# Performance work log

Measured on AMD Instinct MI355X. Metric: run time of the kernel, lower is better.

Reference implementation:

```python
import jax, jax.numpy as jnp
import numpy as np
import math

B, Hdim, Wdim, C = 8, 64, 64, 512
T, TXT = 77, 512
NH, HD = 8, 64  # num_heads, head_dim
TOP_M = 3
CLAMP_LOGIT = 2.0
CONF_THRESH = 0.35
NEG_INF = -1e30


def _ln(x, g, b, eps=1e-5):
    mu = x.mean(-1, keepdims=True)
    var = ((x - mu) ** 2).mean(-1, keepdims=True)
    return (x - mu) * jax.lax.rsqrt(var + eps) * g + b


def _l2norm(x, eps=1e-6):
    n = jnp.sqrt((x * x).sum(-1, keepdims=True))
    return x / jnp.maximum(n, eps)


def setup_inputs() -> dict:
    key = jax.random.key(0)
    ks = jax.random.split(key, 16)
    s = 0.02
    inp = {
        'visual_features': jax.random.normal(ks[0], (B, Hdim, Wdim, C), jnp.float32),
        'text_features': jax.random.normal(ks[1], (B, T, TXT), jnp.float32),
        'ln1_g': jnp.ones((C,), jnp.float32), 'ln1_b': jnp.zeros((C,), jnp.float32),
        'ln2_g': jnp.ones((C,), jnp.float32), 'ln2_b': jnp.zeros((C,), jnp.float32),
        'Wq': jax.random.normal(ks[2], (C, C), jnp.float32) * s, 'bq': jnp.zeros((C,), jnp.float32),
        'Wk': jax.random.normal(ks[3], (TXT, C), jnp.float32) * s, 'bk': jnp.zeros((C,), jnp.float32),
        'Wv': jax.random.normal(ks[4], (TXT, C), jnp.float32) * s, 'bv': jnp.zeros((C,), jnp.float32),
        'Wo': jax.random.normal(ks[5], (C, C), jnp.float32) * s, 'bo': jnp.zeros((C,), jnp.float32),
        'Wg': jax.random.normal(ks[6], (C, 1), jnp.float32) * s, 'bg': jnp.zeros((1,), jnp.float32),
        'W1': jax.random.normal(ks[7], (C, 4 * C), jnp.float32) * s, 'b1': jnp.zeros((4 * C,), jnp.float32),
        'W2': jax.random.normal(ks[8], (4 * C, C), jnp.float32) * s, 'b2': jnp.zeros((C,), jnp.float32),
        'logit_scale': jnp.asarray(math.log(1.0 / 0.07), jnp.float32),
        'alpha': jnp.asarray(0.1, jnp.float32),
    }
    return inp


def reference(visual_features, text_features, ln1_g, ln1_b, ln2_g, ln2_b,
              Wq, bq, Wk, bk, Wv, bv, Wo, bo, Wg, bg, W1, b1, W2, b2,
              logit_scale, alpha):
    b, h, w, c = visual_features.shape
    n = h * w
    # Pre-LN on visual tokens
    x = _ln(visual_features, ln1_g, ln1_b).reshape(b, n, c)
    q_full = x @ Wq + bq                                   # [B,N,C]
    pad_mask = jnp.abs(text_features).sum(-1) <= 1e-6      # [B,T]
    k_full = text_features @ Wk + bk                       # [B,T,C]
    v_full = text_features @ Wv + bv
    # l2-normalize over full channel dim, then split heads
    q = _l2norm(q_full).reshape(b, n, NH, HD)
    k = _l2norm(k_full).reshape(b, T, NH, HD)
    v = v_full.reshape(b, T, NH, HD)
    scale = jnp.exp(jnp.clip(logit_scale, -CLAMP_LOGIT, CLAMP_LOGIT)) / math.sqrt(float(HD))
    sim = jnp.einsum('bnhd,bthd->bnht', q, k) * scale      # [B,N,H,T]
    sim = jnp.where(pad_mask[:, None, None, :], NEG_INF, sim)
    # top-k sparsification: keep top_m per (b,n,h) row
    topv = jax.lax.top_k(sim, TOP_M)[0][..., -1:]
    sim = jnp.where(sim >= topv, sim, NEG_INF)
    attn = jax.nn.softmax(sim, axis=-1)
    attn = attn / jnp.maximum(attn.sum(-1, keepdims=True), 1e-6)
    all_pad = pad_mask.all(axis=1)                         # [B]
    attn = jnp.where(all_pad[:, None, None, None], 0.0, attn)
    # confidence: max-prob * (1 - normalized entropy), mean over heads
    attn_hn = attn.transpose(0, 2, 1, 3)                   # [B,H,N,T]
    maxp = attn_hn.max(-1, keepdims=True)
    t_eff = jnp.maximum((attn_hn > 0).astype(jnp.float32).sum(-1, keepdims=True), 2.0)
    p = jnp.maximum(attn_hn, 1e-8)
    entropy = jnp.maximum(-(p * jnp.log(p)).sum(-1, keepdims=True) / jnp.log(t_eff), 0.0)
    conf = jnp.clip(maxp * (1.0 - entropy), 0.0, 1.0).mean(axis=1)  # [B,N,1]
    bypass = (conf >= CONF_THRESH).astype(attn.dtype)
    aligned = jnp.einsum('bnht,bthd->bnhd', attn, v).reshape(b, n, c)
    aligned = (aligned @ Wo + bo) * bypass
    gate = jax.nn.sigmoid(x @ Wg + bg)                     # [B,N,1]
    y = x + alpha * gate * aligned
    y = _ln(y, ln2_g, ln2_b)
    y = y + (jax.nn.gelu(y @ W1 + b1, approximate=False) @ W2 + b2)
    return y.reshape(b, h, w, c)
```

## Files before the change

### kernel.cpp

```cpp
#include <hip/hip_runtime.h>
#include <stdint.h>

#define BATCH 8
#define NTOK 4096
#define CDIM 512
#define TTXT 77
#define TPAD 80
#define NHEAD 8
#define HDIM 64
#define HID 2048
#define MROWS 32768
#define NEGINF (-1e30f)

typedef __attribute__((ext_vector_type(8))) short short8;
typedef __attribute__((ext_vector_type(4))) float f32x4;

__device__ __forceinline__ float b2f(unsigned short u) {
    union { unsigned int i; float f; } x; x.i = ((unsigned int)u) << 16; return x.f;
}
__device__ __forceinline__ unsigned short f2b(float f) {
    union { float f; unsigned int i; } x; x.f = f;
    unsigned int i = x.i;
    return (unsigned short)((i + 0x7fffu + ((i >> 16) & 1u)) >> 16);
}

__device__ __forceinline__ void gload16(const void* g, void* l) {
    __builtin_amdgcn_global_load_lds(
        (const __attribute__((address_space(1))) unsigned int*)g,
        (__attribute__((address_space(3))) unsigned int*)l, 16, 0, 0);
}

#define OFF_WQT   ((size_t)0)
#define OFF_WKT   (OFF_WQT + 512*512*2)
#define OFF_WVT   (OFF_WKT + 512*512*2)
#define OFF_WOT   (OFF_WVT + 512*512*2)
#define OFF_W1T   (OFF_WOT + 512*512*2)
#define OFF_W2T   (OFF_W1T + (size_t)2048*512*2)
#define OFF_TEXTB (OFF_W2T + (size_t)512*2048*2)
#define OFF_KFB   (OFF_TEXTB + (size_t)640*512*2)
#define OFF_KNRM  (OFF_KFB + (size_t)640*512*2)
#define OFF_VPAD  (OFF_KNRM + (size_t)640*512*2)
#define OFF_PADM  (OFF_VPAD + (size_t)640*512*2)
#define OFF_ALLP  (OFF_PADM + 2560)
#define OFF_GATE  (OFF_ALLP + 256)
#define OFF_BYP   (OFF_GATE + (size_t)MROWS*4)
#define OFF_XB    (OFF_BYP + (size_t)MROWS*4)
#define OFF_BUFB  (OFF_XB + (size_t)MROWS*CDIM*2)
#define OFF_BUFC  (OFF_BUFB + (size_t)MROWS*CDIM*2)
#define OFF_H     (OFF_BUFC + (size_t)MROWS*CDIM*2)
#define WS_NEED   (OFF_H + (size_t)MROWS*HID*2)
#define OFF_VT    OFF_H

__device__ __forceinline__ float waveReduceAdd(float v) {
#pragma unroll
    for (int m = 1; m < 64; m <<= 1) v += __shfl_xor(v, m);
    return v;
}
__device__ __forceinline__ float waveReduceMin(float v) {
#pragma unroll
    for (int m = 1; m < 64; m <<= 1) v = fminf(v, __shfl_xor(v, m));
    return v;
}
__device__ __forceinline__ float red16Max(float v) {
#pragma unroll
    for (int m = 1; m < 16; m <<= 1) v = fmaxf(v, __shfl_xor(v, m));
    return v;
}
__device__ __forceinline__ float red16Add(float v) {
#pragma unroll
    for (int m = 1; m < 16; m <<= 1) v += __shfl_xor(v, m);
    return v;
}

__global__ __launch_bounds__(256) void transpose_kernel(
    const float* __restrict__ in, unsigned short* __restrict__ out, int R, int C)
{
    __shared__ float tile[32][33];
    const int tx = threadIdx.x & 31, ty = threadIdx.x >> 5;
    const int c0 = blockIdx.x * 32, r0 = blockIdx.y * 32;
#pragma unroll
    for (int i = 0; i < 32; i += 8)
        tile[ty + i][tx] = in[(size_t)(r0 + ty + i) * C + c0 + tx];
    __syncthreads();
#pragma unroll
    for (int i = 0; i < 32; i += 8)
        out[(size_t)(c0 + ty + i) * R + r0 + tx] = f2b(tile[tx][ty + i]);
}

__global__ __launch_bounds__(128) void text_prep_kernel(
    const float* __restrict__ text, unsigned short* __restrict__ textb, float* __restrict__ padm)
{
    __shared__ float sred[2];
    const int r = blockIdx.x;
    const int b = r / TPAD, t = r % TPAD;
    const int tid = threadIdx.x;
    if (t < TTXT) {
        float4 v = *(const float4*)(text + ((size_t)(b * TTXT + t)) * 512 + tid * 4);
        float a = fabsf(v.x) + fabsf(v.y) + fabsf(v.z) + fabsf(v.w);
        a = waveReduceAdd(a);
        if ((tid & 63) == 0) sred[tid >> 6] = a;
        __syncthreads();
        float asum = sred[0] + sred[1];
        ushort4 o; o.x = f2b(v.x); o.y = f2b(v.y); o.z = f2b(v.z); o.w = f2b(v.w);
        *(ushort4*)(textb + (size_t)r * 512 + tid * 4) = o;
        if (tid == 0) padm[r] = (asum <= 1e-6f) ? 1.f : 0.f;
    } else {
        ushort4 z; z.x = 0; z.y = 0; z.z = 0; z.w = 0;
        *(ushort4*)(textb + (size_t)r * 512 + tid * 4) = z;
        if (tid == 0) padm[r] = 1.f;
    }
}

__global__ __launch_bounds__(128) void allpad_kernel(
    const float* __restrict__ padm, float* __restrict__ allp)
{
    __shared__ float sred[2];
    const int b = blockIdx.x, tid = threadIdx.x;
    float f = (tid < TTXT) ? padm[b * TPAD + tid] : 1.f;
    f = waveReduceMin(f);
    if ((tid & 63) == 0) sred[tid >> 6] = f;
    __syncthreads();
    if (tid == 0) allp[b] = fminf(sred[0], sred[1]);
}

__global__ __launch_bounds__(128) void ln1_gate_kernel(
    const float* __restrict__ vin, const float* __restrict__ g1, const float* __restrict__ b1v,
    const float* __restrict__ Wg, const float* __restrict__ bg,
    unsigned short* __restrict__ xb, float* __restrict__ gate)
{
    __shared__ float sred[4];
    const int row = blockIdx.x, tid = threadIdx.x;
    const float4 v = *(const float4*)(vin + (size_t)row * 512 + tid * 4);
    float s = v.x + v.y + v.z + v.w;
    float s2 = v.x * v.x + v.y * v.y + v.z * v.z + v.w * v.w;
    s = waveReduceAdd(s); s2 = waveReduceAdd(s2);
    if ((tid & 63) == 0) { sred[tid >> 6] = s; sred[2 + (tid >> 6)] = s2; }
    __syncthreads();
    s = sred[0] + sred[1]; s2 = sred[2] + sred[3];
    const float mu = s * (1.f / 512.f);
    float var = s2 * (1.f / 512.f) - mu * mu;
    const float rs = rsqrtf(fmaxf(var, 0.f) + 1e-5f);
    const float4 gg = *(const float4*)(g1 + tid * 4);
    const float4 bb = *(const float4*)(b1v + tid * 4);
    const float x0 = (v.x - mu) * rs * gg.x + bb.x;
    const float x1 = (v.y - mu) * rs * gg.y + bb.y;
    const float x2 = (v.z - mu) * rs * gg.z + bb.z;
    const float x3 = (v.w - mu) * rs * gg.w + bb.w;
    ushort4 o; o.x = f2b(x0); o.y = f2b(x1); o.z = f2b(x2); o.w = f2b(x3);
    *(ushort4*)(xb + (size_t)row * 512 + tid * 4) = o;
    const float4 wg = *(const float4*)(Wg + tid * 4);
    float gp = x0 * wg.x + x1 * wg.y + x2 * wg.z + x3 * wg.w;
    gp = waveReduceAdd(gp);
    __syncthreads();
    if ((tid & 63) == 0) sred[tid >> 6] = gp;
    __syncthreads();
    if (tid == 0) {
        float z = sred[0] + sred[1] + bg[0];
        gate[row] = 1.f / (1.f + __expf(-z));
    }
}

__global__ __launch_bounds__(128) void ln2_kernel(
    const unsigned short* __restrict__ yin, const float* __restrict__ g2, const float* __restrict__ b2v,
    unsigned short* __restrict__ yb)
{
    __shared__ float sred[4];
    const int row = blockIdx.x, tid = threadIdx.x;
    ushort4 u = *(const ushort4*)(yin + (size_t)row * 512 + tid * 4);
    float v0 = b2f(u.x), v1 = b2f(u.y), v2 = b2f(u.z), v3 = b2f(u.w);
    float s = v0 + v1 + v2 + v3;
    float s2 = v0 * v0 + v1 * v1 + v2 * v2 + v3 * v3;
    s = waveReduceAdd(s); s2 = waveReduceAdd(s2);
    if ((tid & 63) == 0) { sred[tid >> 6] = s; sred[2 + (tid >> 6)] = s2; }
    __syncthreads();
    s = sred[0] + sred[1]; s2 = sred[2] + sred[3];
    const float mu = s * (1.f / 512.f);
    float var = s2 * (1.f / 512.f) - mu * mu;
    const float rs = rsqrtf(fmaxf(var, 0.f) + 1e-5f);
    const float4 gg = *(const float4*)(g2 + tid * 4);
    const float4 bb = *(const float4*)(b2v + tid * 4);
    ushort4 o;
    o.x = f2b((v0 - mu) * rs * gg.x + bb.x);
    o.y = f2b((v1 - mu) * rs * gg.y + bb.y);
    o.z = f2b((v2 - mu) * rs * gg.z + bb.z);
    o.w = f2b((v3 - mu) * rs * gg.w + bb.w);
    *(ushort4*)(yb + (size_t)row * 512 + tid * 4) = o;
}

__global__ __launch_bounds__(128) void l2norm_kernel(
    const unsigned short* __restrict__ in, unsigned short* __restrict__ out)
{
    __shared__ float sred[2];
    const int row = blockIdx.x, tid = threadIdx.x;
    ushort4 u = *(const ushort4*)(in + (size_t)row * 512 + tid * 4);
    float v0 = b2f(u.x), v1 = b2f(u.y), v2 = b2f(u.z), v3 = b2f(u.w);
    float ss = v0 * v0 + v1 * v1 + v2 * v2 + v3 * v3;
    ss = waveReduceAdd(ss);
    if ((tid & 63) == 0) sred[tid >> 6] = ss;
    __syncthreads();
    ss = sred[0] + sred[1];
    const float inv = 1.f / fmaxf(sqrtf(ss), 1e-6f);
    ushort4 o;
    o.x = f2b(v0 * inv); o.y = f2b(v1 * inv); o.z = f2b(v2 * inv); o.w = f2b(v3 * inv);
    *(ushort4*)(out + (size_t)row * 512 + tid * 4) = o;
}

__global__ __launch_bounds__(256) void vt_prep_kernel(
    const unsigned short* __restrict__ vp, unsigned short* __restrict__ vt)
{
    __shared__ unsigned short st[80][72];
    const int b = blockIdx.x >> 3, h = blockIdx.x & 7;
    const int tid = threadIdx.x;
    for (int idx = tid; idx < 80 * 64; idx += 256) {
        int t = idx >> 6, d = idx & 63;
        st[t][d] = vp[((size_t)(b * TPAD + t)) * 512 + h * 64 + d];
    }
    __syncthreads();
    for (int idx = tid; idx < 64 * 96; idx += 256) {
        int d = idx / 96, t = idx - d * 96;
        vt[((size_t)blockIdx.x * 64 + d) * 96 + t] = (t < TPAD) ? st[t][d] : (unsigned short)0;
    }
}

__global__ __launch_bounds__(256) void gemm_bt(
    const unsigned short* __restrict__ A, const unsigned short* __restrict__ Bt,
    const float* __restrict__ bias,
    unsigned short* __restrict__ outb, int M, int N, int K)
{
    __shared__ unsigned short sA[128 * 64];
    __shared__ unsigned short sB[128 * 64];
    char* cA = (char*)sA;
    char* cB = (char*)sB;
    const int tid = threadIdx.x;
    const int lane = tid & 63, w = tid >> 6;
    const int g = lane >> 4, ln = lane & 15;
    const int WR = w >> 1, WC = w & 1;
    const int rowA0 = blockIdx.x * 128, colB0 = blockIdx.y * 128;

    f32x4 acc[4][4];
#pragma unroll
    for (int m = 0; m < 4; ++m)
#pragma unroll
        for (int n = 0; n < 4; ++n) acc[m][n] = (f32x4){0.f, 0.f, 0.f, 0.f};

    for (int k0 = 0; k0 < K; k0 += 64) {
        __syncthreads();
#pragma unroll
        for (int i = 0; i < 4; ++i) {
            int c = tid + i * 256;
            int row = c >> 3, kc = c & 7;
            int kcs = kc ^ (row & 7);
            gload16(A + (size_t)(rowA0 + row) * K + k0 + kcs * 8, cA + c * 16);
            gload16(Bt + (size_t)(colB0 + row) * K + k0 + kcs * 8, cB + c * 16);
        }
        __syncthreads();
#pragma unroll
        for (int kk = 0; kk < 2; ++kk) {
            short8 af[4], bf[4];
#pragma unroll
            for (int m = 0; m < 4; ++m) {
                int row = WR * 64 + m * 16 + ln;
                af[m] = *(const short8*)(cA + row * 128 + ((kk * 64 + g * 16) ^ ((row & 7) << 4)));
            }
#pragma unroll
            for (int n = 0; n < 4; ++n) {
                int col = WC * 64 + n * 16 + ln;
                bf[n] = *(const short8*)(cB + col * 128 + ((kk * 64 + g * 16) ^ ((col & 7) << 4)));
            }
#pragma unroll
            for (int m = 0; m < 4; ++m)
#pragma unroll
                for (int n = 0; n < 4; ++n)
                    acc[m][n] = __builtin_amdgcn_mfma_f32_16x16x32_bf16(af[m], bf[n], acc[m][n], 0, 0, 0);
        }
    }

#pragma unroll
    for (int m = 0; m < 4; ++m) {
        const int rbase = rowA0 + WR * 64 + m * 16 + g * 4;
#pragma unroll
        for (int n = 0; n < 4; ++n) {
            const int col = colB0 + WC * 64 + n * 16 + ln;
            const float bcol = bias[col];
#pragma unroll
            for (int i = 0; i < 4; ++i)
                outb[(size_t)(rbase + i) * N + col] = f2b(acc[m][n][i] + bcol);
        }
    }
}

template<int EPI>
__global__ __launch_bounds__(512, 2) void gemm256(
    const unsigned short* __restrict__ A, const unsigned short* __restrict__ Bt,
    const float* __restrict__ bias,
    unsigned short* __restrict__ outb, float* __restrict__ outf,
    int M, int N, int K,
    const unsigned short* __restrict__ xres, const float* __restrict__ gate,
    const float* __restrict__ byp, const unsigned short* __restrict__ yres,
    const float* __restrict__ alphaPtr, int gxM, int gyN)
{
    __shared__ unsigned short lds[2][2][16384];
    const int tid = threadIdx.x;
    const int lane = tid & 63, w = tid >> 6;
    const int g = lane >> 4, ln = lane & 15;
    const int wr = w >> 2, wc = w & 3;

    int bm, bn;
    {
        const int L = (int)blockIdx.x;
        const int xcd = L & 7, j = L >> 3;
        const int rl = j / gyN;
        bn = j - rl * gyN;
        bm = xcd * (gxM >> 3) + rl;
    }
    const int rowA0 = bm * 256, colB0 = bn * 256;
    const int nt = K >> 6;

    auto stageA = [&](int t, int mh) {
        const int buf = t & 1;
#pragma unroll
        for (int r = 0; r < 2; ++r) {
            const int c = tid + r * 512;
            const int prl = c >> 3, kc = c & 7;
            const int grow = rowA0 + ((prl >> 6) << 7) + (mh << 6) + (prl & 63);
            gload16(A + (size_t)grow * K + (t << 6) + ((kc ^ (prl & 7)) << 3),
                    (char*)&lds[buf][0][mh * 8192] + c * 16);
        }
    };
    auto stageB = [&](int t, int nh) {
        const int buf = t & 1;
#pragma unroll
        for (int r = 0; r < 2; ++r) {
            const int c = tid + r * 512;
            const int prl = c >> 3, kc = c & 7;
            const int gcol = colB0 + ((prl >> 5) << 6) + (nh << 5) + (prl & 31);
            gload16(Bt + (size_t)gcol * K + (t << 6) + ((kc ^ (prl & 7)) << 3),
                    (char*)&lds[buf][1][nh * 8192] + c * 16);
        }
    };

    f32x4 acc[8][4];
#pragma unroll
    for (int m = 0; m < 8; ++m)
#pragma unroll
        for (int n = 0; n < 4; ++n) acc[m][n] = (f32x4){0.f, 0.f, 0.f, 0.f};

    stageA(0, 0); stageB(0, 0); stageB(0, 1); stageA(0, 1);
    stageA(1, 0); stageB(1, 0); stageB(1, 1);
    asm volatile("s_waitcnt vmcnt(6)" ::: "memory");
    __builtin_amdgcn_s_barrier();

    const int sw  = (ln & 7) << 4;
    const int kb0 = (g * 16) ^ sw;
    const int kb1 = (64 + g * 16) ^ sw;
    const int arow = (wr * 64 + ln) * 128;
    const int brow = (wc * 32 + ln) * 128;

    short8 afr[4][2], bfr[4][2];

    for (int t = 0; t < nt; ++t) {
        const char* lA = (const char*)&lds[t & 1][0][0];
        const char* lB = (const char*)&lds[t & 1][1][0];

#pragma unroll
        for (int m = 0; m < 4; ++m) {
            afr[m][0] = *(const short8*)(lA + arow + m * 2048 + kb0);
            afr[m][1] = *(const short8*)(lA + arow + m * 2048 + kb1);
        }
#pragma unroll
        for (int n = 0; n < 2; ++n) {
            bfr[n][0] = *(const short8*)(lB + brow + n * 2048 + kb0);
            bfr[n][1] = *(const short8*)(lB + brow + n * 2048 + kb1);
        }
        if (t + 1 < nt) stageA(t + 1, 1);
        __builtin_amdgcn_s_barrier();
        __builtin_amdgcn_s_setprio(1);
#pragma unroll
        for (int m = 0; m < 4; ++m)
#pragma unroll
            for (int n = 0; n < 2; ++n) {
                acc[m][n] = __builtin_amdgcn_mfma_f32_16x16x32_bf16(afr[m][0], bfr[n][0], acc[m][n], 0, 0, 0);
                acc[m][n] = __builtin_amdgcn_mfma_f32_16x16x32_bf16(afr[m][1], bfr[n][1], acc[m][n], 0, 0, 0);
            }
        __builtin_amdgcn_s_setprio(0);
        __builtin_amdgcn_s_barrier();

#pragma unroll
        for (int n = 2; n < 4; ++n) {
            bfr[n][0] = *(const short8*)(lB + brow + (n & 1) * 2048 + 16384 + kb0);
            bfr[n][1] = *(const short8*)(lB + brow + (n & 1) * 2048 + 16384 + kb1);
        }
        if (t + 2 < nt) stageA(t + 2, 0);
        __builtin_amdgcn_s_barrier();
        __builtin_amdgcn_s_setprio(1);
#pragma unroll
        for (int m = 0; m < 4; ++m)
#pragma unroll
            for (int n = 2; n < 4; ++n) {
                acc[m][n] = __builtin_amdgcn_mfma_f32_16x16x32_bf16(afr[m][0], bfr[n][0], acc[m][n], 0, 0, 0);
                acc[m][n] = __builtin_amdgcn_mfma_f32_16x16x32_bf16(afr[m][1], bfr[n][1], acc[m][n], 0, 0, 0);
            }
        __builtin_amdgcn_s_setprio(0);
        __builtin_amdgcn_s_barrier();

#pragma unroll
        for (int m = 0; m < 4; ++m) {
            afr[m][0] = *(const short8*)(lA + arow + m * 2048 + 16384 + kb0);
            afr[m][1] = *(const short8*)(lA + arow + m * 2048 + 16384 + kb1);
        }
        if (t + 2 < nt) stageB(t + 2, 0);
        __builtin_amdgcn_s_barrier();
        __builtin_amdgcn_s_setprio(1);
#pragma unroll
        for (int m = 0; m < 4; ++m)
#pragma unroll
            for (int n = 0; n < 2; ++n) {
                acc[m + 4][n] = __builtin_amdgcn_mfma_f32_16x16x32_bf16(afr[m][0], bfr[n][0], acc[m + 4][n], 0, 0, 0);
                acc[m + 4][n] = __builtin_amdgcn_mfma_f32_16x16x32_bf16(afr[m][1], bfr[n][1], acc[m + 4][n], 0, 0, 0);
            }
        __builtin_amdgcn_s_setprio(0);
        __builtin_amdgcn_s_barrier();

        if (t + 2 < nt) stageB(t + 2, 1);
        if (t == nt - 2) { asm volatile("s_waitcnt vmcnt(0)" ::: "memory"); }
        else             { asm volatile("s_waitcnt vmcnt(6)" ::: "memory"); }
        __builtin_amdgcn_s_barrier();
        __builtin_amdgcn_s_setprio(1);
#pragma unroll
        for (int m = 0; m < 4; ++m)
#pragma unroll
            for (int n = 2; n < 4; ++n) {
                acc[m + 4][n] = __builtin_amdgcn_mfma_f32_16x16x32_bf16(afr[m][0], bfr[n][0], acc[m + 4][n], 0, 0, 0);
                acc[m + 4][n] = __builtin_amdgcn_mfma_f32_16x16x32_bf16(afr[m][1], bfr[n][1], acc[m + 4][n], 0, 0, 0);
            }
        __builtin_amdgcn_s_setprio(0);
        __builtin_amdgcn_s_barrier();
    }

    const float alpha = (EPI == 1) ? *alphaPtr : 0.f;
#pragma unroll
    for (int m = 0; m < 8; ++m) {
        const int rbase = rowA0 + wr * 128 + m * 16 + g * 4;
#pragma unroll
        for (int n = 0; n < 4; ++n) {
            const int col = colB0 + wc * 64 + n * 16 + ln;
            const float bcol = bias[col];
#pragma unroll
            for (int i = 0; i < 4; ++i) {
                const int row = rbase + i;
                const float v = acc[m][n][i] + bcol;
                if (EPI == 0) {
                    outb[(size_t)row * N + col] = f2b(v);
                } else if (EPI == 1) {
                    float yp = b2f(xres[(size_t)row * N + col]) + alpha * gate[row] * byp[row] * v;
                    outb[(size_t)row * N + col] = f2b(yp);
                } else if (EPI == 2) {
                    const float u2 = 2.f * v * (0.7978845608f + 0.0356774081f * v * v);
                    const float tt = 1.f - 2.f / (__expf(u2) + 1.f);
                    outb[(size_t)row * N + col] = f2b(0.5f * v * (1.f + tt));
                } else {
                    outf[(size_t)row * N + col] = b2f(yres[(size_t)row * N + col]) + v;
                }
            }
        }
    }
}

__global__ __launch_bounds__(256) void attn_kernel(
    const unsigned short* __restrict__ qn,
    const unsigned short* __restrict__ kn,
    const unsigned short* __restrict__ vt,
    const float* __restrict__ padm,
    const float* __restrict__ allp,
    const float* __restrict__ lscPtr,
    unsigned short* __restrict__ aligned,
    float* __restrict__ bypass)
{
    const int b = blockIdx.y;
    const int n0 = blockIdx.x * 16;
    const int tid = threadIdx.x;
    const int w = tid >> 6, lane = tid & 63, g = lane >> 4, ln = lane & 15;
    __shared__ unsigned short s_p[4][16][104];
    __shared__ float s_conf[4][16];

    if (allp[b] > 0.5f) {
        uint4 z = {0u, 0u, 0u, 0u};
#pragma unroll
        for (int j = 0; j < 4; ++j) {
            int id = tid + j * 256;
            int row = id >> 6, c8 = id & 63;
            *(uint4*)(aligned + ((size_t)(b * NTOK + n0 + row)) * 512 + c8 * 8) = z;
        }
        if (tid < 16) bypass[b * NTOK + n0 + tid] = 0.f;
        return;
    }

    float lscale;
    {
        float ls = *lscPtr;
        ls = fminf(fmaxf(ls, -2.f), 2.f);
        lscale = __expf(ls) * 0.125f;
    }

    float pm[5];
#pragma unroll
    for (int tt = 0; tt < 5; ++tt) {
        int t = ln + tt * 16;
        pm[tt] = (t < TTXT) ? padm[b * TPAD + t] : 1.f;
    }

    for (int j = g; j < 24; j += 4) s_p[w][ln][80 + j] = 0;

    float conf_acc[4] = {0.f, 0.f, 0.f, 0.f};
    const size_t qrow = ((size_t)(b * NTOK + n0 + ln)) * 512;

#pragma unroll
    for (int hh = 0; hh < 2; ++hh) {
        const int h = w + hh * 4;
        short8 a0 = *(const short8*)(qn + qrow + h * 64 + g * 8);
        short8 a1 = *(const short8*)(qn + qrow + h * 64 + 32 + g * 8);
        f32x4 sim[5];
#pragma unroll
        for (int tt = 0; tt < 5; ++tt) {
            const size_t kbase = ((size_t)(b * TPAD + tt * 16 + ln)) * 512 + h * 64;
            short8 b0 = *(const short8*)(kn + kbase + g * 8);
            short8 b1 = *(const short8*)(kn + kbase + 32 + g * 8);
            f32x4 c = (f32x4){0.f, 0.f, 0.f, 0.f};
            c = __builtin_amdgcn_mfma_f32_16x16x32_bf16(a0, b0, c, 0, 0, 0);
            c = __builtin_amdgcn_mfma_f32_16x16x32_bf16(a1, b1, c, 0, 0, 0);
            sim[tt] = c;
        }
#pragma unroll
        for (int i = 0; i < 4; ++i) {
            float v[5];
#pragma unroll
            for (int tt = 0; tt < 5; ++tt)
                v[tt] = (pm[tt] == 0.f) ? sim[tt][i] * lscale : NEGINF;

            float lm = v[0];
#pragma unroll
            for (int tt = 1; tt < 5; ++tt) lm = fmaxf(lm, v[tt]);
            const float m1 = red16Max(lm);
            float lm2 = -3.0e38f;
#pragma unroll
            for (int tt = 0; tt < 5; ++tt) if (v[tt] < m1) lm2 = fmaxf(lm2, v[tt]);
            const float m2 = red16Max(lm2);
            float lm3 = -3.0e38f;
#pragma unroll
            for (int tt = 0; tt < 5; ++tt) if (v[tt] < m2) lm3 = fmaxf(lm3, v[tt]);
            const float m3 = red16Max(lm3);
            float lc1 = 0.f, lc2 = 0.f;
#pragma unroll
            for (int tt = 0; tt < 5; ++tt) {
                if (v[tt] >= m1) lc1 += 1.f;
                if (v[tt] >= m2) lc2 += 1.f;
            }
            const float c1 = red16Add(lc1);
            const float c2 = red16Add(lc2);
            const float th = (c1 >= 3.f) ? m1 : ((c2 >= 3.f) ? m2 : m3);

            float p[5], lsum = 0.f, lcnt = 0.f;
#pragma unroll
            for (int tt = 0; tt < 5; ++tt) {
                float pv = (v[tt] >= th) ? __expf(v[tt] - m1) : 0.f;
                p[tt] = pv;
                lsum += pv;
                lcnt += (pv > 0.f) ? 1.f : 0.f;
            }
            const float psum = red16Add(lsum);
            const float pcnt = red16Add(lcnt);
            const float inv = 1.f / fmaxf(psum, 1e-20f);

            float lmaxp = 0.f, lent = 0.f;
#pragma unroll
            for (int tt = 0; tt < 5; ++tt) {
                float a = p[tt] * inv;
                p[tt] = a;
                lmaxp = fmaxf(lmaxp, a);
                if (a > 0.f) {
                    float pp = fmaxf(a, 1e-8f);
                    lent += -pp * __logf(pp);
                }
            }
            const float maxp = red16Max(lmaxp);
            float ent = red16Add(lent);
            ent += (77.f - pcnt) * 1.8420680744e-7f;
            const float teff = fmaxf(pcnt, 2.f);
            const float entropy = fmaxf(ent / __logf(teff), 0.f);
            const float confh = fminf(fmaxf(maxp * (1.f - entropy), 0.f), 1.f);
            conf_acc[i] += confh;

#pragma unroll
            for (int tt = 0; tt < 5; ++tt)
                s_p[w][g * 4 + i][ln + tt * 16] = f2b(p[tt]);
        }
        short8 af[3];
#pragma unroll
        for (int k = 0; k < 3; ++k)
            af[k] = *(const short8*)(&s_p[w][ln][k * 32 + g * 8]);
        const size_t vtb = ((size_t)(b * NHEAD + h)) * 64;
#pragma unroll
        for (int n = 0; n < 4; ++n) {
            f32x4 o = (f32x4){0.f, 0.f, 0.f, 0.f};
#pragma unroll
            for (int k = 0; k < 3; ++k) {
                short8 bf = *(const short8*)(vt + (vtb + n * 16 + ln) * 96 + k * 32 + g * 8);
                o = __builtin_amdgcn_mfma_f32_16x16x32_bf16(af[k], bf, o, 0, 0, 0);
            }
#pragma unroll
            for (int i = 0; i < 4; ++i)
                aligned[((size_t)(b * NTOK + n0 + g * 4 + i)) * 512 + h * 64 + n * 16 + ln] =
                    f2b(o[i]);
        }
    }

    if (ln == 0) {
#pragma unroll
        for (int i = 0; i < 4; ++i) s_conf[w][g * 4 + i] = conf_acc[i];
    }
    __syncthreads();
    if (tid < 16) {
        float c = (s_conf[0][tid] + s_conf[1][tid] + s_conf[2][tid] + s_conf[3][tid]) * 0.125f;
        bypass[b * NTOK + n0 + tid] = (c >= 0.35f) ? 1.f : 0.f;
    }
}

extern "C" void kernel_launch(void* const* d_in, const int* in_sizes, int n_in,
                              void* d_out, int out_size, void* d_ws, size_t ws_size,
                              hipStream_t stream)
{
    (void)in_sizes; (void)n_in; (void)out_size;
    if (ws_size < WS_NEED) return;

    const float* visual = (const float*)d_in[0];
    const float* text   = (const float*)d_in[1];
    const float* ln1_g  = (const float*)d_in[2];
    const float* ln1_b  = (const float*)d_in[3];
    const float* ln2_g  = (const float*)d_in[4];
    const float* ln2_b  = (const float*)d_in[5];
    const float* Wq = (const float*)d_in[6];   const float* bq = (const float*)d_in[7];
    const float* Wk = (const float*)d_in[8];   const float* bk = (const float*)d_in[9];
    const float* Wv = (const float*)d_in[10];  const float* bv = (const float*)d_in[11];
    const float* Wo = (const float*)d_in[12];  const float* bo = (const float*)d_in[13];
    const float* Wg = (const float*)d_in[14];  const float* bg = (const float*)d_in[15];
    const float* W1 = (const float*)d_in[16];  const float* b1 = (const float*)d_in[17];
    const float* W2 = (const float*)d_in[18];  const float* b2 = (const float*)d_in[19];
    const float* lsc = (const float*)d_in[20];
    const float* alp = (const float*)d_in[21];

    char* ws = (char*)d_ws;
    unsigned short* WQT  = (unsigned short*)(ws + OFF_WQT);
    unsigned short* WKT  = (unsigned short*)(ws + OFF_WKT);
    unsigned short* WVT  = (unsigned short*)(ws + OFF_WVT);
    unsigned short* WOT  = (unsigned short*)(ws + OFF_WOT);
    unsigned short* W1T  = (unsigned short*)(ws + OFF_W1T);
    unsigned short* W2T  = (unsigned short*)(ws + OFF_W2T);
    unsigned short* TEXTB = (unsigned short*)(ws + OFF_TEXTB);
    unsigned short* KFB  = (unsigned short*)(ws + OFF_KFB);
    unsigned short* KNRM = (unsigned short*)(ws + OFF_KNRM);
    unsigned short* VPAD = (unsigned short*)(ws + OFF_VPAD);
    float* PADM = (float*)(ws + OFF_PADM);
    float* ALLP = (float*)(ws + OFF_ALLP);
    float* GATE = (float*)(ws + OFF_GATE);
    float* BYP  = (float*)(ws + OFF_BYP);
    unsigned short* XB   = (unsigned short*)(ws + OFF_XB);
    unsigned short* BUFB = (unsigned short*)(ws + OFF_BUFB);
    unsigned short* BUFC = (unsigned short*)(ws + OFF_BUFC);
    unsigned short* HBUF = (unsigned short*)(ws + OFF_H);
    unsigned short* VT   = (unsigned short*)(ws + OFF_VT);
    float* out = (float*)d_out;

    transpose_kernel<<<dim3(16, 16), 256, 0, stream>>>(Wq, WQT, 512, 512);
    transpose_kernel<<<dim3(16, 16), 256, 0, stream>>>(Wk, WKT, 512, 512);
    transpose_kernel<<<dim3(16, 16), 256, 0, stream>>>(Wv, WVT, 512, 512);
    transpose_kernel<<<dim3(16, 16), 256, 0, stream>>>(Wo, WOT, 512, 512);
    transpose_kernel<<<dim3(64, 16), 256, 0, stream>>>(W1, W1T, 512, 2048);
    transpose_kernel<<<dim3(16, 64), 256, 0, stream>>>(W2, W2T, 2048, 512);

    text_prep_kernel<<<640, 128, 0, stream>>>(text, TEXTB, PADM);
    allpad_kernel<<<BATCH, 128, 0, stream>>>(PADM, ALLP);

    ln1_gate_kernel<<<MROWS, 128, 0, stream>>>(visual, ln1_g, ln1_b, Wg, bg, XB, GATE);

    gemm_bt<<<dim3(5, 4), 256, 0, stream>>>(TEXTB, WKT, bk, KFB, 640, 512, 512);
    gemm_bt<<<dim3(5, 4), 256, 0, stream>>>(TEXTB, WVT, bv, VPAD, 640, 512, 512);
    l2norm_kernel<<<640, 128, 0, stream>>>(KFB, KNRM);
    vt_prep_kernel<<<BATCH * NHEAD, 256, 0, stream>>>(VPAD, VT);

    gemm256<0><<<dim3(128 * 2), 512, 0, stream>>>(XB, WQT, bq, BUFB, nullptr, MROWS, 512, 512,
                                                  nullptr, nullptr, nullptr, nullptr, nullptr,
                                                  128, 2);
    l2norm_kernel<<<MROWS, 128, 0, stream>>>(BUFB, BUFC);

    attn_kernel<<<dim3(NTOK / 16, BATCH), 256, 0, stream>>>(BUFC, KNRM, VT, PADM, ALLP, lsc,
                                                            BUFB, BYP);

    gemm256<1><<<dim3(128 * 2), 512, 0, stream>>>(BUFB, WOT, bo, BUFC, nullptr, MROWS, 512, 512,
                                                  XB, GATE, BYP, nullptr, alp, 128, 2);

    ln2_kernel<<<MROWS, 128, 0, stream>>>(BUFC, ln2_g, ln2_b, XB);

    gemm256<2><<<dim3(128 * 8), 512, 0, stream>>>(XB, W1T, b1, HBUF, nullptr, MROWS, HID, 512,
                                                  nullptr, nullptr, nullptr, nullptr, nullptr,
                                                  128, 8);
    gemm256<3><<<dim3(128 * 2), 512, 0, stream>>>(HBUF, W2T, b2, nullptr, out, MROWS, 512, HID,
                                                  nullptr, nullptr, nullptr, XB, nullptr,
                                                  128, 2);
}
```

Measured before the change: 398.5 us.

## Fuse query L2-norm into attention kernel and merge weight transposes

```diff
diff --git a/kernel.cpp b/kernel.cpp
--- a/kernel.cpp
+++ b/kernel.cpp
@@ -72,19 +72,34 @@
     return v;
 }
 
-__global__ __launch_bounds__(256) void transpose_kernel(
-    const float* __restrict__ in, unsigned short* __restrict__ out, int R, int C)
+__global__ __launch_bounds__(256) void transpose_all_kernel(
+    const float* __restrict__ Wq, const float* __restrict__ Wk,
+    const float* __restrict__ Wv, const float* __restrict__ Wo,
+    const float* __restrict__ W1, const float* __restrict__ W2,
+    unsigned short* __restrict__ WQT, unsigned short* __restrict__ WKT,
+    unsigned short* __restrict__ WVT, unsigned short* __restrict__ WOT,
+    unsigned short* __restrict__ W1T, unsigned short* __restrict__ W2T)
 {
     __shared__ float tile[32][33];
+    int b = blockIdx.x;
+    const float* src; unsigned short* dst; int R, C, cx, ry;
+    if (b < 1024)       { src = W1; dst = W1T; R = 512;  C = 2048; cx = b & 63; ry = b >> 6; }
+    else if (b < 2048)  { b -= 1024; src = W2; dst = W2T; R = 2048; C = 512; cx = b & 15; ry = b >> 4; }
+    else {
+        b -= 2048; const int which = b >> 8; b &= 255;
+        R = 512; C = 512; cx = b & 15; ry = b >> 4;
+        src = (which == 0) ? Wq : (which == 1) ? Wk : (which == 2) ? Wv : Wo;
+        dst = (which == 0) ? WQT : (which == 1) ? WKT : (which == 2) ? WVT : WOT;
+    }
     const int tx = threadIdx.x & 31, ty = threadIdx.x >> 5;
-    const int c0 = blockIdx.x * 32, r0 = blockIdx.y * 32;
+    const int c0 = cx * 32, r0 = ry * 32;
 #pragma unroll
     for (int i = 0; i < 32; i += 8)
-        tile[ty + i][tx] = in[(size_t)(r0 + ty + i) * C + c0 + tx];
+        tile[ty + i][tx] = src[(size_t)(r0 + ty + i) * C + c0 + tx];
     __syncthreads();
 #pragma unroll
     for (int i = 0; i < 32; i += 8)
-        out[(size_t)(c0 + ty + i) * R + r0 + tx] = f2b(tile[tx][ty + i]);
+        dst[(size_t)(c0 + ty + i) * R + r0 + tx] = f2b(tile[tx][ty + i]);
 }
 
 __global__ __launch_bounds__(128) void text_prep_kernel(
@@ -482,6 +497,7 @@
     const int w = tid >> 6, lane = tid & 63, g = lane >> 4, ln = lane & 15;
     __shared__ unsigned short s_p[4][16][104];
     __shared__ float s_conf[4][16];
+    __shared__ float s_inv[16];
 
     if (allp[b] > 0.5f) {
         uint4 z = {0u, 0u, 0u, 0u};
@@ -493,6 +509,23 @@
         }
         if (tid < 16) bypass[b * NTOK + n0 + tid] = 0.f;
         return;
+    }
+
+    {
+        const int r = tid >> 4, seg = tid & 15;
+        const unsigned short* qp = qn + ((size_t)(b * NTOK + n0 + r)) * 512 + seg * 32;
+        float ss = 0.f;
+#pragma unroll
+        for (int j = 0; j < 4; ++j) {
+            short8 u = *(const short8*)(qp + j * 8);
+#pragma unroll
+            for (int e = 0; e < 8; ++e) {
+                float f = b2f(((const unsigned short*)&u)[e]);
+                ss += f * f;
+            }
+        }
+        ss = red16Add(ss);
+        if (seg == 0) s_inv[r] = 1.f / fmaxf(sqrtf(ss), 1e-6f);
     }
 
     float lscale;
@@ -510,6 +543,7 @@
     }
 
     for (int j = g; j < 24; j += 4) s_p[w][ln][80 + j] = 0;
+    __syncthreads();
 
     float conf_acc[4] = {0.f, 0.f, 0.f, 0.f};
     const size_t qrow = ((size_t)(b * NTOK + n0 + ln)) * 512;
@@ -532,10 +566,11 @@
         }
 #pragma unroll
         for (int i = 0; i < 4; ++i) {
+            const float qs = lscale * s_inv[g * 4 + i];
             float v[5];
 #pragma unroll
             for (int tt = 0; tt < 5; ++tt)
-                v[tt] = (pm[tt] == 0.f) ? sim[tt][i] * lscale : NEGINF;
+                v[tt] = (pm[tt] == 0.f) ? sim[tt][i] * qs : NEGINF;
 
             float lm = v[0];
 #pragma unroll
@@ -670,12 +705,8 @@
     unsigned short* VT   = (unsigned short*)(ws + OFF_VT);
     float* out = (float*)d_out;
 
-    transpose_kernel<<<dim3(16, 16), 256, 0, stream>>>(Wq, WQT, 512, 512);
-    transpose_kernel<<<dim3(16, 16), 256, 0, stream>>>(Wk, WKT, 512, 512);
-    transpose_kernel<<<dim3(16, 16), 256, 0, stream>>>(Wv, WVT, 512, 512);
-    transpose_kernel<<<dim3(16, 16), 256, 0, stream>>>(Wo, WOT, 512, 512);
-    transpose_kernel<<<dim3(64, 16), 256, 0, stream>>>(W1, W1T, 512, 2048);
-    transpose_kernel<<<dim3(16, 64), 256, 0, stream>>>(W2, W2T, 2048, 512);
+    transpose_all_kernel<<<3072, 256, 0, stream>>>(Wq, Wk, Wv, Wo, W1, W2,
+                                                   WQT, WKT, WVT, WOT, W1T, W2T);
 
     text_prep_kernel<<<640, 128, 0, stream>>>(text, TEXTB, PADM);
     allpad_kernel<<<BATCH, 128, 0, stream>>>(PADM, ALLP);
@@ -690,15 +721,14 @@
     gemm256<0><<<dim3(128 * 2), 512, 0, stream>>>(XB, WQT, bq, BUFB, nullptr, MROWS, 512, 512,
                                                   nullptr, nullptr, nullptr, nullptr, nullptr,
                                                   128, 2);
-    l2norm_kernel<<<MROWS, 128, 0, stream>>>(BUFB, BUFC);
-
-    attn_kernel<<<dim3(NTOK / 16, BATCH), 256, 0, stream>>>(BUFC, KNRM, VT, PADM, ALLP, lsc,
-                                                            BUFB, BYP);
-
-    gemm256<1><<<dim3(128 * 2), 512, 0, stream>>>(BUFB, WOT, bo, BUFC, nullptr, MROWS, 512, 512,
+
+    attn_kernel<<<dim3(NTOK / 16, BATCH), 256, 0, stream>>>(BUFB, KNRM, VT, PADM, ALLP, lsc,
+                                                            BUFC, BYP);
+
+    gemm256<1><<<dim3(128 * 2), 512, 0, stream>>>(BUFC, WOT, bo, BUFB, nullptr, MROWS, 512, 512,
                                                   XB, GATE, BYP, nullptr, alp, 128, 2);
 
-    ln2_kernel<<<MROWS, 128, 0, stream>>>(BUFC, ln2_g, ln2_b, XB);
+    ln2_kernel<<<MROWS, 128, 0, stream>>>(BUFB, ln2_g, ln2_b, XB);
 
     gemm256<2><<<dim3(128 * 8), 512, 0, stream>>>(XB, W1T, b1, HBUF, nullptr, MROWS, HID, 512,
                                                   nullptr, nullptr, nullptr, nullptr, nullptr,
```

Result: faster. 380.1 us (-4.6%).
